# Kernel tuning notes

Hardware: AMD Instinct MI355X
Metric: run time of the kernel (lower is better)

The kernel has to match this reference:

```python
import jax, jax.numpy as jnp
import numpy as np

D_MODEL = 1024
NUM_HEADS = 16
D_K = D_MODEL // NUM_HEADS


def setup_inputs() -> dict:
    key = jax.random.key(0)
    k_x, k_q, k_k, k_v, k_o = jax.random.split(key, 5)
    s = 1.0 / np.sqrt(D_MODEL)
    return {
        "x": jax.random.normal(k_x, (2, 2048, D_MODEL), dtype=jnp.float32),
        "W_q": jax.random.normal(k_q, (D_MODEL, D_MODEL), dtype=jnp.float32) * s,
        "W_k": jax.random.normal(k_k, (D_MODEL, D_MODEL), dtype=jnp.float32) * s,
        "W_v": jax.random.normal(k_v, (D_MODEL, D_MODEL), dtype=jnp.float32) * s,
        "W_o": jax.random.normal(k_o, (D_MODEL, D_MODEL), dtype=jnp.float32) * s,
    }


def reference(x, W_q, W_k, W_v, W_o):
    B, S, D = x.shape
    H, dk = NUM_HEADS, D_K
    # nn.Linear(y) = y @ W.T ; weights stored as (out, in)
    def proj(W):
        return (x @ W.T).reshape(B, S, H, dk).transpose(0, 2, 1, 3)  # (B,H,S,dk)
    Q, K, V = proj(W_q), proj(W_k), proj(W_v)
    scores = jnp.einsum("bhqd,bhkd->bhqk", Q, K) / np.sqrt(dk)  # (B,H,S,S)
    attn = jax.nn.softmax(scores, axis=-1)
    out = jnp.einsum("bhqk,bhkd->bhqd", attn, V)  # (B,H,S,dk)
    out = out.transpose(0, 2, 1, 3).reshape(B, S, D)
    return out @ W_o.T
```

## Files before the change

kernel.cpp:

```cpp
#include <hip/hip_runtime.h>
#include <hip/hip_bf16.h>

#define SEQ 2048
#define DM  1024
#define NH  16
#define DK  64
#define MROWS 4096

typedef __attribute__((ext_vector_type(8))) short short8;
typedef __attribute__((ext_vector_type(4))) short short4v;
typedef __attribute__((ext_vector_type(4))) float float4v;
typedef __attribute__((ext_vector_type(2))) unsigned uint2v;

__device__ __forceinline__ short f2bf(float f) {
  union { float f; unsigned u; } v; v.f = f;
  unsigned r = v.u + 0x7fffu + ((v.u >> 16) & 1u);
  return (short)(r >> 16);
}

#if __has_builtin(__builtin_amdgcn_exp2f)
#define EXP2(x) __builtin_amdgcn_exp2f(x)
#else
#define EXP2(x) exp2f(x)
#endif

__device__ __forceinline__ unsigned pack_bfu(float a, float b) {
  unsigned ua = __float_as_uint(a) + 0x8000u;
  unsigned ub = __float_as_uint(b) + 0x8000u;
#if __has_builtin(__builtin_amdgcn_perm)
  return __builtin_amdgcn_perm(ub, ua, 0x07060302u);
#else
  return (ua >> 16) | (ub & 0xffff0000u);
#endif
}

__global__ __launch_bounds__(256) void cvt_kernel(
    const float* __restrict__ in, short* __restrict__ out) {
  int i = blockIdx.x * 256 + threadIdx.x;
  float4v f = ((const float4v*)in)[i];
  short4v s;
#pragma unroll
  for (int j = 0; j < 4; ++j) s[j] = f2bf(f[j]);
  ((short4v*)out)[i] = s;
}

__global__ __launch_bounds__(256) void cvt4_kernel(
    const float* __restrict__ a, const float* __restrict__ b,
    const float* __restrict__ c, const float* __restrict__ d,
    short* __restrict__ out) {
  const float* srcs[4] = {a, b, c, d};
  const float* s = srcs[blockIdx.y];
  int i = blockIdx.x * 256 + threadIdx.x;
  float4v f = ((const float4v*)s)[i];
  short4v sv;
#pragma unroll
  for (int j = 0; j < 4; ++j) sv[j] = f2bf(f[j]);
  ((short4v*)(out + (size_t)blockIdx.y * DM * DM))[i] = sv;
}

template<int WM, int WN, typename TC>
__global__ __launch_bounds__(WM*WN*64, 3) void gemm_bt(
    const short* __restrict__ A, const short* __restrict__ Bw0,
    TC* __restrict__ C0, int M, int N, int K, size_t strB, size_t strC,
    short* __restrict__ vtOut, float qs0)
{
  constexpr int THREADS = WM * WN * 64;
  constexpr int TM = WM * 64, TN = WN * 64;
  constexpr int CA = TM * 64 / (8 * THREADS);
  constexpr int CB = TN * 64 / (8 * THREADS);
  __shared__ __align__(16) short SMEM[(TM + TN) * 72];
  short* Al = SMEM;
  short* Bl = SMEM + TM * 72;

  const short* Bw = Bw0 + (size_t)blockIdx.z * strB;
  TC* C = C0 + (size_t)blockIdx.z * strC;

  const int tid  = threadIdx.x;
  const int lane = tid & 63, wave = tid >> 6;
  const int l16  = lane & 15, quad = lane >> 4;
  const int wm   = (wave / WN) * 64, wn = (wave % WN) * 64;
  const int cm   = blockIdx.y * TM, cn = blockIdx.x * TN;

  float4v acc[4][4];
#pragma unroll
  for (int i = 0; i < 4; ++i)
#pragma unroll
    for (int j = 0; j < 4; ++j)
#pragma unroll
      for (int r = 0; r < 4; ++r) acc[i][j][r] = 0.f;

  const short* ag = A  + (size_t)cm * K;
  const short* bg = Bw + (size_t)cn * K;
  int rwa[CA], rwb[CB];
#pragma unroll
  for (int i = 0; i < CA; ++i) rwa[i] = (i * THREADS + tid) >> 3;
#pragma unroll
  for (int i = 0; i < CB; ++i) rwb[i] = (i * THREADS + tid) >> 3;
  const int cl = (tid & 7) * 8;

  short8 ra[CA], rb[CB];
  auto loadG = [&](int k0) {
#pragma unroll
    for (int i = 0; i < CA; ++i)
      ra[i] = *(const short8*)(ag + (size_t)rwa[i] * K + k0 + cl);
#pragma unroll
    for (int i = 0; i < CB; ++i)
      rb[i] = *(const short8*)(bg + (size_t)rwb[i] * K + k0 + cl);
  };
  auto writeL = [&]() {
#pragma unroll
    for (int i = 0; i < CA; ++i) *(short8*)&Al[rwa[i] * 72 + cl] = ra[i];
#pragma unroll
    for (int i = 0; i < CB; ++i) *(short8*)&Bl[rwb[i] * 72 + cl] = rb[i];
  };
  auto compute = [&]() {
#pragma unroll
    for (int ks = 0; ks < 2; ++ks) {
      short8 af[4], bfr[4];
#pragma unroll
      for (int mi = 0; mi < 4; ++mi)
        af[mi] = *(const short8*)&Al[(wm + mi*16 + l16) * 72 + ks*32 + quad*8];
#pragma unroll
      for (int ni = 0; ni < 4; ++ni)
        bfr[ni] = *(const short8*)&Bl[(wn + ni*16 + l16) * 72 + ks*32 + quad*8];
#pragma unroll
      for (int mi = 0; mi < 4; ++mi)
#pragma unroll
        for (int ni = 0; ni < 4; ++ni)
          acc[mi][ni] = __builtin_amdgcn_mfma_f32_16x16x32_bf16(
              af[mi], bfr[ni], acc[mi][ni], 0, 0, 0);
    }
  };

  loadG(0);
  writeL();
  __syncthreads();
  for (int k0 = 0; k0 < K; k0 += 64) {
    bool nxt = (k0 + 64 < K);
    if (nxt) loadG(k0 + 64);
    compute();
    __syncthreads();
    if (nxt) { writeL(); __syncthreads(); }
  }

  const float scl = (blockIdx.z == 0) ? qs0 : 1.f;

  if constexpr (WM == 2 && WN == 2) {
    if (vtOut != nullptr && blockIdx.z == 2) {
      short* T = SMEM;
#pragma unroll
      for (int mi = 0; mi < 4; ++mi)
#pragma unroll
        for (int ni = 0; ni < 4; ++ni)
#pragma unroll
          for (int r = 0; r < 4; ++r)
            T[(wn + ni*16 + l16) * 136 + wm + mi*16 + quad*4 + r] =
                f2bf(acc[mi][ni][r]);
      __syncthreads();
      const int nrow = tid >> 1, mo = (tid & 1) * 64;
      const int b = cm >> 11;
      const int s0 = (cm & (SEQ - 1)) + mo;
      short* vt = vtOut + ((size_t)b * DM + cn + nrow) * SEQ + s0;
#pragma unroll
      for (int j = 0; j < 8; ++j)
        *(short8*)(vt + j * 8) = *(const short8*)&T[nrow * 136 + mo + j * 8];
      return;
    }
  }
#pragma unroll
  for (int mi = 0; mi < 4; ++mi)
#pragma unroll
    for (int ni = 0; ni < 4; ++ni)
#pragma unroll
      for (int r = 0; r < 4; ++r) {
        int m = cm + wm + mi*16 + quad*4 + r;
        int n = cn + wn + ni*16 + l16;
        float v = acc[mi][ni][r] * scl;
        if constexpr (sizeof(TC) == 2) C[(size_t)m * N + n] = f2bf(v);
        else                           C[(size_t)m * N + n] = v;
      }
}

__global__ __launch_bounds__(256) void flash_kernel(
    const short* __restrict__ Q, const short* __restrict__ Kg,
    const short* __restrict__ VTg, short* __restrict__ AO)
{
  __shared__ __align__(16) short Kl[2][64 * 72];
  __shared__ __align__(16) short Vt[2][64 * 72];
  __shared__ __align__(16) short Pl[4][32 * 72];
  __shared__ float lsumL[4][32];
  const int tid  = threadIdx.x;
  const int lane = tid & 63, wave = tid >> 6;
  const int l16  = lane & 15, quad = lane >> 4;
  const int q0   = blockIdx.x * 128;
  const int hc   = blockIdx.y * DK;
  const size_t base = (size_t)blockIdx.z * SEQ;

  short8 qfr[2][2];
#pragma unroll
  for (int qf = 0; qf < 2; ++qf)
#pragma unroll
    for (int ks = 0; ks < 2; ++ks)
      qfr[qf][ks] = *(const short8*)(Q + (base + q0 + wave*32 + qf*16 + l16) * DM
                                     + hc + ks*32 + quad*8);

  float4v O[2][4];
  float lsum[2] = {0.f, 0.f};
#pragma unroll
  for (int mt = 0; mt < 2; ++mt)
#pragma unroll
    for (int nt = 0; nt < 4; ++nt)
#pragma unroll
      for (int r = 0; r < 4; ++r) O[mt][nt][r] = 0.f;

  const float4v z4 = {0.f, 0.f, 0.f, 0.f};

  const int r0 = tid >> 3, r1 = (256 + tid) >> 3;
  const int c0 = (tid & 7) * 8;
  const short* vtb = VTg + ((size_t)blockIdx.z * DM + hc) * SEQ;

  short8 ka0, ka1, va0, va1;
  auto loadKV = [&](int kb) {
    ka0 = *(const short8*)(Kg + (base + kb*64 + r0) * DM + hc + c0);
    ka1 = *(const short8*)(Kg + (base + kb*64 + r1) * DM + hc + c0);
    va0 = *(const short8*)(vtb + (size_t)r0 * SEQ + kb*64 + c0);
    va1 = *(const short8*)(vtb + (size_t)r1 * SEQ + kb*64 + c0);
  };
  auto writeKV = [&](int buf) {
    *(short8*)&Kl[buf][r0 * 72 + c0] = ka0;
    *(short8*)&Kl[buf][r1 * 72 + c0] = ka1;
    *(short8*)&Vt[buf][r0 * 72 + c0] = va0;
    *(short8*)&Vt[buf][r1 * 72 + c0] = va1;
  };

  loadKV(0);
  writeKV(0);
  __syncthreads();

  int cur = 0;
  for (int kb = 0; kb < SEQ / 64; ++kb) {
    bool nxt = (kb + 1 < SEQ / 64);
    if (nxt) loadKV(kb + 1);

    float4v s[4][2];
#pragma unroll
    for (int kf = 0; kf < 4; ++kf) {
      short8 k0 = *(const short8*)&Kl[cur][(kf*16 + l16) * 72 + quad*8];
      short8 k1 = *(const short8*)&Kl[cur][(kf*16 + l16) * 72 + 32 + quad*8];
#pragma unroll
      for (int qf = 0; qf < 2; ++qf) {
        float4v t = __builtin_amdgcn_mfma_f32_16x16x32_bf16(k0, qfr[qf][0], z4, 0, 0, 0);
        s[kf][qf]  = __builtin_amdgcn_mfma_f32_16x16x32_bf16(k1, qfr[qf][1], t, 0, 0, 0);
      }
    }
#pragma unroll
    for (int kf = 0; kf < 4; ++kf)
#pragma unroll
      for (int qf = 0; qf < 2; ++qf) {
        float p0 = EXP2(s[kf][qf][0]), p1 = EXP2(s[kf][qf][1]);
        float p2 = EXP2(s[kf][qf][2]), p3 = EXP2(s[kf][qf][3]);
        lsum[qf] += (p0 + p1) + (p2 + p3);
        uint2v pk;
        pk[0] = pack_bfu(p0, p1);
        pk[1] = pack_bfu(p2, p3);
        *(uint2v*)&Pl[wave][(qf*16 + l16) * 72 + kf*16 + quad*4] = pk;
      }
#pragma unroll
    for (int ks = 0; ks < 2; ++ks) {
      short8 pf[2];
#pragma unroll
      for (int mt = 0; mt < 2; ++mt)
        pf[mt] = *(const short8*)&Pl[wave][(mt*16 + l16) * 72 + ks*32 + quad*8];
#pragma unroll
      for (int nt = 0; nt < 4; ++nt) {
        short8 vf = *(const short8*)&Vt[cur][(nt*16 + l16) * 72 + ks*32 + quad*8];
#pragma unroll
        for (int mt = 0; mt < 2; ++mt)
          O[mt][nt] = __builtin_amdgcn_mfma_f32_16x16x32_bf16(
              pf[mt], vf, O[mt][nt], 0, 0, 0);
      }
    }
    if (nxt) writeKV(cur ^ 1);
    __syncthreads();
    cur ^= 1;
  }

#pragma unroll
  for (int qf = 0; qf < 2; ++qf) {
    float l = lsum[qf];
    l += __shfl_xor(l, 16, 64);
    l += __shfl_xor(l, 32, 64);
    lsumL[wave][qf*16 + l16] = l;
  }
#pragma unroll
  for (int mt = 0; mt < 2; ++mt) {
    float inv[4];
#pragma unroll
    for (int r = 0; r < 4; ++r)
      inv[r] = 1.f / lsumL[wave][mt*16 + quad*4 + r];
#pragma unroll
    for (int nt = 0; nt < 4; ++nt)
#pragma unroll
      for (int r = 0; r < 4; ++r) {
        int m = q0 + wave*32 + mt*16 + quad*4 + r;
        AO[(base + m) * DM + hc + nt*16 + l16] = f2bf(O[mt][nt][r] * inv[r]);
      }
  }
}

extern "C" void kernel_launch(void* const* d_in, const int* in_sizes, int n_in,
                              void* d_out, int out_size, void* d_ws, size_t ws_size,
                              hipStream_t stream) {
  (void)in_sizes; (void)n_in; (void)out_size; (void)ws_size;
  const float* x  = (const float*)d_in[0];
  const float* Wq = (const float*)d_in[1];
  const float* Wk = (const float*)d_in[2];
  const float* Wv = (const float*)d_in[3];
  const float* Wo = (const float*)d_in[4];
  float* out = (float*)d_out;

  const size_t NX = (size_t)MROWS * DM;
  const size_t NW = (size_t)DM * DM;
  short* xb  = (short*)d_ws;
  short* Wqb = xb  + NX;
  short* Qb  = Wqb + 4 * NW;
  short* Kb  = Qb  + NX;
  short* AO  = Kb  + NX;
  short* VTb = AO  + NX;

  cvt_kernel<<<dim3(NX / 4 / 256), 256, 0, stream>>>(x, xb);
  cvt4_kernel<<<dim3(NW / 4 / 256, 4), 256, 0, stream>>>(Wq, Wk, Wv, Wo, Wqb);

  const float qs = 0.18033688011112042f;

  gemm_bt<2, 2, short><<<dim3(DM / 128, MROWS / 128, 3), 256, 0, stream>>>(
      xb, Wqb, Qb, MROWS, DM, DM, NW, NX, VTb, qs);

  flash_kernel<<<dim3(SEQ / 128, NH, 2), 256, 0, stream>>>(Qb, Kb, VTb, AO);

  gemm_bt<1, 2, float><<<dim3(DM / 128, MROWS / 64, 1), 128, 0, stream>>>(
      AO, Wqb + 3 * NW, out, MROWS, DM, DM, 0, 0, nullptr, 1.f);
}
```

Baseline: 203.4 us.

## Stage GEMM and attention tiles via direct global-to-LDS loads with XOR swizzle

Replaces the register-staged global loads and LDS writes in the GEMM and flash-attention kernels with global_load_lds direct copies. Padded LDS rows are replaced by an XOR-swizzled unpadded layout to avoid bank conflicts. The GEMM loses its register prefetch and now loads then syncs each k-step, so global latency is no longer overlapped with compute there. It also reorders the flash grid so heads vary fastest, sets an occupancy hint on the flash kernel, and gives the output projection four narrower waves per block.

```diff
diff --git a/kernel.cpp b/kernel.cpp
--- a/kernel.cpp
+++ b/kernel.cpp
@@ -11,6 +11,13 @@
 typedef __attribute__((ext_vector_type(4))) short short4v;
 typedef __attribute__((ext_vector_type(4))) float float4v;
 typedef __attribute__((ext_vector_type(2))) unsigned uint2v;
+
+typedef const __attribute__((address_space(1))) unsigned gu32;
+typedef __attribute__((address_space(3))) unsigned lu32;
+
+__device__ __forceinline__ void gl2lds16(const void* g, void* l) {
+  __builtin_amdgcn_global_load_lds((gu32*)g, (lu32*)l, 16, 0, 0);
+}
 
 __device__ __forceinline__ short f2bf(float f) {
   union { float f; unsigned u; } v; v.f = f;
@@ -58,19 +65,20 @@
   ((short4v*)(out + (size_t)blockIdx.y * DM * DM))[i] = sv;
 }
 
-template<int WM, int WN, typename TC>
-__global__ __launch_bounds__(WM*WN*64, 3) void gemm_bt(
+template<int WMW, int WNW, int WNSZ, typename TC>
+__global__ __launch_bounds__(WMW*WNW*64, 3) void gemm_bt(
     const short* __restrict__ A, const short* __restrict__ Bw0,
     TC* __restrict__ C0, int M, int N, int K, size_t strB, size_t strC,
     short* __restrict__ vtOut, float qs0)
 {
-  constexpr int THREADS = WM * WN * 64;
-  constexpr int TM = WM * 64, TN = WN * 64;
+  constexpr int WAVES = WMW * WNW, THREADS = WAVES * 64;
+  constexpr int TM = WMW * 64, TN = WNW * WNSZ, NI = WNSZ / 16;
   constexpr int CA = TM * 64 / (8 * THREADS);
   constexpr int CB = TN * 64 / (8 * THREADS);
-  __shared__ __align__(16) short SMEM[(TM + TN) * 72];
+  constexpr int SM_SZ = (WMW == 2 && WNW == 2) ? 128 * 136 : (TM + TN) * 64;
+  __shared__ __align__(16) short SMEM[SM_SZ];
   short* Al = SMEM;
-  short* Bl = SMEM + TM * 72;
+  short* Bl = SMEM + TM * 64;
 
   const short* Bw = Bw0 + (size_t)blockIdx.z * strB;
   TC* C = C0 + (size_t)blockIdx.z * strC;
@@ -78,74 +86,66 @@
   const int tid  = threadIdx.x;
   const int lane = tid & 63, wave = tid >> 6;
   const int l16  = lane & 15, quad = lane >> 4;
-  const int wm   = (wave / WN) * 64, wn = (wave % WN) * 64;
+  const int wm   = (wave / WNW) * 64, wn = (wave % WNW) * WNSZ;
   const int cm   = blockIdx.y * TM, cn = blockIdx.x * TN;
 
-  float4v acc[4][4];
+  float4v acc[4][NI];
 #pragma unroll
   for (int i = 0; i < 4; ++i)
 #pragma unroll
-    for (int j = 0; j < 4; ++j)
+    for (int j = 0; j < NI; ++j)
 #pragma unroll
       for (int r = 0; r < 4; ++r) acc[i][j][r] = 0.f;
 
   const short* ag = A  + (size_t)cm * K;
   const short* bg = Bw + (size_t)cn * K;
-  int rwa[CA], rwb[CB];
-#pragma unroll
-  for (int i = 0; i < CA; ++i) rwa[i] = (i * THREADS + tid) >> 3;
-#pragma unroll
-  for (int i = 0; i < CB; ++i) rwb[i] = (i * THREADS + tid) >> 3;
-  const int cl = (tid & 7) * 8;
-
-  short8 ra[CA], rb[CB];
-  auto loadG = [&](int k0) {
-#pragma unroll
-    for (int i = 0; i < CA; ++i)
-      ra[i] = *(const short8*)(ag + (size_t)rwa[i] * K + k0 + cl);
-#pragma unroll
-    for (int i = 0; i < CB; ++i)
-      rb[i] = *(const short8*)(bg + (size_t)rwb[i] * K + k0 + cl);
-  };
-  auto writeL = [&]() {
-#pragma unroll
-    for (int i = 0; i < CA; ++i) *(short8*)&Al[rwa[i] * 72 + cl] = ra[i];
-#pragma unroll
-    for (int i = 0; i < CB; ++i) *(short8*)&Bl[rwb[i] * 72 + cl] = rb[i];
+
+  auto stage = [&](int k0) {
+#pragma unroll
+    for (int i = 0; i < CA; ++i) {
+      int c = i * THREADS + tid;
+      int row = c >> 3, cg = (c & 7) ^ (row & 7);
+      gl2lds16(ag + (size_t)row * K + k0 + cg * 8,
+               &Al[(i * WAVES + wave) * 512]);
+    }
+#pragma unroll
+    for (int i = 0; i < CB; ++i) {
+      int c = i * THREADS + tid;
+      int row = c >> 3, cg = (c & 7) ^ (row & 7);
+      gl2lds16(bg + (size_t)row * K + k0 + cg * 8,
+               &Bl[(i * WAVES + wave) * 512]);
+    }
   };
   auto compute = [&]() {
 #pragma unroll
     for (int ks = 0; ks < 2; ++ks) {
-      short8 af[4], bfr[4];
+      const int sw = ((ks * 4 + quad) ^ (l16 & 7)) << 3;
+      short8 af[4], bfr[NI];
 #pragma unroll
       for (int mi = 0; mi < 4; ++mi)
-        af[mi] = *(const short8*)&Al[(wm + mi*16 + l16) * 72 + ks*32 + quad*8];
-#pragma unroll
-      for (int ni = 0; ni < 4; ++ni)
-        bfr[ni] = *(const short8*)&Bl[(wn + ni*16 + l16) * 72 + ks*32 + quad*8];
+        af[mi] = *(const short8*)&Al[(wm + mi*16 + l16) * 64 + sw];
+#pragma unroll
+      for (int ni = 0; ni < NI; ++ni)
+        bfr[ni] = *(const short8*)&Bl[(wn + ni*16 + l16) * 64 + sw];
 #pragma unroll
       for (int mi = 0; mi < 4; ++mi)
 #pragma unroll
-        for (int ni = 0; ni < 4; ++ni)
+        for (int ni = 0; ni < NI; ++ni)
           acc[mi][ni] = __builtin_amdgcn_mfma_f32_16x16x32_bf16(
               af[mi], bfr[ni], acc[mi][ni], 0, 0, 0);
     }
   };
 
-  loadG(0);
-  writeL();
-  __syncthreads();
   for (int k0 = 0; k0 < K; k0 += 64) {
-    bool nxt = (k0 + 64 < K);
-    if (nxt) loadG(k0 + 64);
+    stage(k0);
+    __syncthreads();
     compute();
     __syncthreads();
-    if (nxt) { writeL(); __syncthreads(); }
   }
 
   const float scl = (blockIdx.z == 0) ? qs0 : 1.f;
 
-  if constexpr (WM == 2 && WN == 2) {
+  if constexpr (WMW == 2 && WNW == 2) {
     if (vtOut != nullptr && blockIdx.z == 2) {
       short* T = SMEM;
 #pragma unroll
@@ -170,7 +170,7 @@
 #pragma unroll
   for (int mi = 0; mi < 4; ++mi)
 #pragma unroll
-    for (int ni = 0; ni < 4; ++ni)
+    for (int ni = 0; ni < NI; ++ni)
 #pragma unroll
       for (int r = 0; r < 4; ++r) {
         int m = cm + wm + mi*16 + quad*4 + r;
@@ -181,19 +181,19 @@
       }
 }
 
-__global__ __launch_bounds__(256) void flash_kernel(
+__global__ __launch_bounds__(256, 3) void flash_kernel(
     const short* __restrict__ Q, const short* __restrict__ Kg,
     const short* __restrict__ VTg, short* __restrict__ AO)
 {
-  __shared__ __align__(16) short Kl[2][64 * 72];
-  __shared__ __align__(16) short Vt[2][64 * 72];
-  __shared__ __align__(16) short Pl[4][32 * 72];
+  __shared__ __align__(16) short Kl[2][64 * 64];
+  __shared__ __align__(16) short Vt[2][64 * 64];
+  __shared__ __align__(16) short Pl[4][32 * 64];
   __shared__ float lsumL[4][32];
   const int tid  = threadIdx.x;
   const int lane = tid & 63, wave = tid >> 6;
   const int l16  = lane & 15, quad = lane >> 4;
-  const int q0   = blockIdx.x * 128;
-  const int hc   = blockIdx.y * DK;
+  const int hc   = blockIdx.x * DK;
+  const int q0   = blockIdx.y * 128;
   const size_t base = (size_t)blockIdx.z * SEQ;
 
   short8 qfr[2][2];
@@ -214,39 +214,34 @@
       for (int r = 0; r < 4; ++r) O[mt][nt][r] = 0.f;
 
   const float4v z4 = {0.f, 0.f, 0.f, 0.f};
-
-  const int r0 = tid >> 3, r1 = (256 + tid) >> 3;
-  const int c0 = (tid & 7) * 8;
   const short* vtb = VTg + ((size_t)blockIdx.z * DM + hc) * SEQ;
 
-  short8 ka0, ka1, va0, va1;
-  auto loadKV = [&](int kb) {
-    ka0 = *(const short8*)(Kg + (base + kb*64 + r0) * DM + hc + c0);
-    ka1 = *(const short8*)(Kg + (base + kb*64 + r1) * DM + hc + c0);
-    va0 = *(const short8*)(vtb + (size_t)r0 * SEQ + kb*64 + c0);
-    va1 = *(const short8*)(vtb + (size_t)r1 * SEQ + kb*64 + c0);
+  auto stageKV = [&](int buf, int kb) {
+#pragma unroll
+    for (int i = 0; i < 2; ++i) {
+      int c = i * 256 + tid;
+      int row = c >> 3, cg = (c & 7) ^ (row & 7);
+      gl2lds16(Kg + (base + kb*64 + row) * DM + hc + cg * 8,
+               &Kl[buf][(i * 4 + wave) * 512]);
+      gl2lds16(vtb + (size_t)row * SEQ + kb*64 + cg * 8,
+               &Vt[buf][(i * 4 + wave) * 512]);
+    }
   };
-  auto writeKV = [&](int buf) {
-    *(short8*)&Kl[buf][r0 * 72 + c0] = ka0;
-    *(short8*)&Kl[buf][r1 * 72 + c0] = ka1;
-    *(short8*)&Vt[buf][r0 * 72 + c0] = va0;
-    *(short8*)&Vt[buf][r1 * 72 + c0] = va1;
-  };
-
-  loadKV(0);
-  writeKV(0);
+
+  stageKV(0, 0);
   __syncthreads();
 
   int cur = 0;
   for (int kb = 0; kb < SEQ / 64; ++kb) {
     bool nxt = (kb + 1 < SEQ / 64);
-    if (nxt) loadKV(kb + 1);
+    if (nxt) stageKV(cur ^ 1, kb + 1);
 
     float4v s[4][2];
 #pragma unroll
     for (int kf = 0; kf < 4; ++kf) {
-      short8 k0 = *(const short8*)&Kl[cur][(kf*16 + l16) * 72 + quad*8];
-      short8 k1 = *(const short8*)&Kl[cur][(kf*16 + l16) * 72 + 32 + quad*8];
+      const int rowb = (kf*16 + l16) * 64;
+      short8 k0 = *(const short8*)&Kl[cur][rowb + ((quad       ^ (l16 & 7)) << 3)];
+      short8 k1 = *(const short8*)&Kl[cur][rowb + (((4 + quad) ^ (l16 & 7)) << 3)];
 #pragma unroll
       for (int qf = 0; qf < 2; ++qf) {
         float4v t = __builtin_amdgcn_mfma_f32_16x16x32_bf16(k0, qfr[qf][0], z4, 0, 0, 0);
@@ -263,24 +258,25 @@
         uint2v pk;
         pk[0] = pack_bfu(p0, p1);
         pk[1] = pack_bfu(p2, p3);
-        *(uint2v*)&Pl[wave][(qf*16 + l16) * 72 + kf*16 + quad*4] = pk;
+        *(uint2v*)&Pl[wave][(qf*16 + l16) * 64 +
+                            ((kf*16 + quad*4) ^ ((l16 & 7) << 3))] = pk;
       }
 #pragma unroll
     for (int ks = 0; ks < 2; ++ks) {
+      const int sw = ((ks*4 + quad) ^ (l16 & 7)) << 3;
       short8 pf[2];
 #pragma unroll
       for (int mt = 0; mt < 2; ++mt)
-        pf[mt] = *(const short8*)&Pl[wave][(mt*16 + l16) * 72 + ks*32 + quad*8];
+        pf[mt] = *(const short8*)&Pl[wave][(mt*16 + l16) * 64 + sw];
 #pragma unroll
       for (int nt = 0; nt < 4; ++nt) {
-        short8 vf = *(const short8*)&Vt[cur][(nt*16 + l16) * 72 + ks*32 + quad*8];
+        short8 vf = *(const short8*)&Vt[cur][(nt*16 + l16) * 64 + sw];
 #pragma unroll
         for (int mt = 0; mt < 2; ++mt)
           O[mt][nt] = __builtin_amdgcn_mfma_f32_16x16x32_bf16(
               pf[mt], vf, O[mt][nt], 0, 0, 0);
       }
     }
-    if (nxt) writeKV(cur ^ 1);
     __syncthreads();
     cur ^= 1;
   }
@@ -333,11 +329,11 @@
 
   const float qs = 0.18033688011112042f;
 
-  gemm_bt<2, 2, short><<<dim3(DM / 128, MROWS / 128, 3), 256, 0, stream>>>(
+  gemm_bt<2, 2, 64, short><<<dim3(DM / 128, MROWS / 128, 3), 256, 0, stream>>>(
       xb, Wqb, Qb, MROWS, DM, DM, NW, NX, VTb, qs);
 
-  flash_kernel<<<dim3(SEQ / 128, NH, 2), 256, 0, stream>>>(Qb, Kb, VTb, AO);
-
-  gemm_bt<1, 2, float><<<dim3(DM / 128, MROWS / 64, 1), 128, 0, stream>>>(
+  flash_kernel<<<dim3(NH, SEQ / 128, 2), 256, 0, stream>>>(Qb, Kb, VTb, AO);
+
+  gemm_bt<1, 4, 32, float><<<dim3(DM / 128, MROWS / 64, 1), 256, 0, stream>>>(
       AO, Wqb + 3 * NW, out, MROWS, DM, DM, 0, 0, nullptr, 1.f);
 }
```

After: 181.8 us. 1.12x faster.
